# Kernel tuning notes

Measured on AMD Instinct MI355X. Metric: run time of the kernel, lower is better.

Reference implementation:

```python
import jax, jax.numpy as jnp
import numpy as np

N_EMBED = 1024
HIDDEN = int(2 / 3 * 4 * N_EMBED)  # 2730, matches SwiGLU default
NUM_EXPERTS = 8
TOP_K = 2


def setup_inputs() -> dict:
    key = jax.random.key(0)
    ks = jax.random.split(key, 5)
    B, T, C, E, H = 2, 2048, N_EMBED, NUM_EXPERTS, HIDDEN
    s = 0.02
    return {
        "x": jax.random.normal(ks[0], (B, T, C), dtype=jnp.float32),
        "gate_w": jax.random.normal(ks[1], (E, C), dtype=jnp.float32) * s,  # Linear(C->E) weight [out,in]
        "w1": jax.random.normal(ks[2], (E, H, C), dtype=jnp.float32) * s,   # per-expert Linear(C->H)
        "w2": jax.random.normal(ks[3], (E, H, C), dtype=jnp.float32) * s,   # per-expert Linear(C->H)
        "w3": jax.random.normal(ks[4], (E, C, H), dtype=jnp.float32) * s,   # per-expert Linear(H->C)
    }


def reference(x, gate_w, w1, w2, w3):
    B, T, C = x.shape
    E = gate_w.shape[0]
    xt = x.reshape(-1, C)                      # [N, C], N = B*T
    N = xt.shape[0]

    # Router: top-k logits, softmax over the selected logits only
    logits = jnp.einsum("nc,ec->ne", xt, gate_w)          # [N, E]
    top_vals, top_idx = jax.lax.top_k(logits, TOP_K)       # [N, K]
    top_w = jax.nn.softmax(top_vals.astype(jnp.float32), axis=-1).astype(x.dtype)

    # Dense routing-weight matrix [N, E] (top-k indices are distinct per token)
    route = jnp.zeros((N, E), dtype=x.dtype)
    route = route.at[jnp.arange(N)[:, None], top_idx].set(top_w)

    # SwiGLU for all experts, batched over the expert axis (faithful math,
    # vectorized instead of the per-expert Python-loop gather/scatter)
    h1 = jnp.einsum("nc,ehc->enh", xt, w1)                 # [E, N, H]
    h2 = jnp.einsum("nc,ehc->enh", xt, w2)                 # [E, N, H]
    act = jax.nn.silu(h1) * h2                              # [E, N, H]
    expert_out = jnp.einsum("enh,ech->enc", act, w3)       # [E, N, C]

    out = jnp.einsum("ne,enc->nc", route, expert_out)      # weighted combine
    return out.reshape(B, T, C)
```

## Files before the change

kernel.cpp:

```cpp
#include <hip/hip_runtime.h>
#include <hip/hip_bf16.h>
#include <cstdint>
#include <cstddef>

#define TOKENS 4096
#define CDIM   1024
#define HDIM   2730
#define HPAD2  2816
#define NEXP   8
#define NPAIR  (TOKENS * 2)
#define NTB1   (HPAD2 / 128)
#define NTB2   (CDIM / 256)
#define NT1    (CDIM / 64)
#define NT2    (HPAD2 / 64)
#define NCONV3 256

typedef __bf16 bf16_t;
typedef bf16_t bf16x8 __attribute__((ext_vector_type(8)));
typedef float  f32x4  __attribute__((ext_vector_type(4)));

static __device__ __forceinline__ unsigned short f2bf(float f) {
    union { float f; unsigned int u; } v; v.f = f;
    unsigned int u = v.u;
    return (unsigned short)((u + 0x7FFFu + ((u >> 16) & 1u)) >> 16);
}
static __device__ __forceinline__ unsigned int pack2(float a, float b) {
    return (unsigned int)f2bf(a) | ((unsigned int)f2bf(b) << 16);
}

typedef __attribute__((address_space(3))) unsigned int lds_uint;
typedef const __attribute__((address_space(1))) unsigned int glob_uint;
static __device__ __forceinline__ void gl_lds16(const void* g, void* l) {
    __builtin_amdgcn_global_load_lds((glob_uint*)g, (lds_uint*)l, 16, 0, 0);
}


__global__ __launch_bounds__(256) void moe_router_zero(
    const float* __restrict__ x, const float* __restrict__ gw,
    int* __restrict__ meta, int* __restrict__ tok_idx, float* __restrict__ tok_w,
    float* __restrict__ out)
{
    if (blockIdx.x >= 1024) {
        int b = blockIdx.x - 1024;
        float4 z4 = {0.f, 0.f, 0.f, 0.f};
#pragma unroll
        for (int i = 0; i < 4; ++i)
            ((float4*)out)[(size_t)b * 1024 + i * 256 + threadIdx.x] = z4;
        return;
    }
    int wave = threadIdx.x >> 6;
    int lane = threadIdx.x & 63;
    int t = blockIdx.x * 4 + wave;

    float acc[NEXP];
#pragma unroll
    for (int e = 0; e < NEXP; ++e) acc[e] = 0.f;

    const float4* xr = (const float4*)(x + (size_t)t * CDIM);
#pragma unroll
    for (int it = 0; it < 4; ++it) {
        int c4 = it * 64 + lane;
        float4 xv = xr[c4];
#pragma unroll
        for (int e = 0; e < NEXP; ++e) {
            float4 gv = ((const float4*)(gw + e * CDIM))[c4];
            acc[e] += xv.x * gv.x + xv.y * gv.y + xv.z * gv.z + xv.w * gv.w;
        }
    }
#pragma unroll
    for (int e = 0; e < NEXP; ++e) {
#pragma unroll
        for (int off = 32; off > 0; off >>= 1)
            acc[e] += __shfl_xor(acc[e], off, 64);
    }
    if (lane == 0) {
        int e0 = 0; float v0 = acc[0];
#pragma unroll
        for (int e = 1; e < NEXP; ++e) if (acc[e] > v0) { v0 = acc[e]; e0 = e; }
        int e1 = -1; float v1 = -3.0e38f;
#pragma unroll
        for (int e = 0; e < NEXP; ++e) if (e != e0 && acc[e] > v1) { v1 = acc[e]; e1 = e; }
        float w0 = 1.f / (1.f + __expf(v1 - v0));
        tok_idx[2 * t] = e0; tok_idx[2 * t + 1] = e1;
        tok_w[2 * t] = w0;  tok_w[2 * t + 1] = 1.f - w0;
        atomicAdd(&meta[e0], 1);
        atomicAdd(&meta[e1], 1);
    }
}

__global__ void moe_scan(int* meta) {
    if (threadIdx.x == 0) {
        int s = 0;
        for (int e = 0; e < NEXP; ++e) { meta[8 + e] = s; s += meta[e]; }
        meta[16] = s;
        int nb1 = 0;
        for (int e = 0; e < NEXP; ++e) {
            int beg = meta[8 + e], end = meta[8 + e] + meta[e];
            for (int m0 = beg; m0 < end; m0 += 256) {
                meta[32 + 2 * nb1] = e;
                meta[33 + 2 * nb1] = m0;
                ++nb1;
            }
        }
        meta[17] = nb1;
    }
}

__global__ __launch_bounds__(256) void moe_scatter(
    const int* __restrict__ tok_idx, const float* __restrict__ tok_w, int* meta,
    int* __restrict__ pair_token, float* __restrict__ pair_w)
{
    int t = blockIdx.x * 256 + threadIdx.x;
    if (t >= TOKENS) return;
#pragma unroll
    for (int k = 0; k < 2; ++k) {
        int e = tok_idx[2 * t + k];
        int pos = atomicAdd(&meta[24 + e], 1);
        int slot = meta[8 + e] + pos;
        pair_token[slot] = t;
        pair_w[slot] = tok_w[2 * t + k];
    }
}

__global__ __launch_bounds__(256) void moe_gather_conv12(
    const float* __restrict__ x, const int* __restrict__ pair_token,
    unsigned short* __restrict__ Xg,
    const float* __restrict__ w1, const float* __restrict__ w2,
    unsigned short* __restrict__ w1b, unsigned short* __restrict__ w2b)
{
    if (blockIdx.x < 1024) {
        int base = blockIdx.x * 8;
        int i = threadIdx.x;
#pragma unroll
        for (int r = 0; r < 8; ++r) {
            int row = base + r;
            int t = pair_token[row];
            float4 v = ((const float4*)(x + (size_t)t * CDIM))[i];
            ushort4 o;
            o.x = f2bf(v.x); o.y = f2bf(v.y); o.z = f2bf(v.z); o.w = f2bf(v.w);
            ((ushort4*)(Xg + (size_t)row * CDIM))[i] = o;
        }
        return;
    }
    int zz = blockIdx.x - 1024;
    int which = zz / 2816;
    int rr = zz - which * 2816;
    int e = rr / 352;
    int blk = rr - e * 352;
    const float* wsrc = which ? w2 : w1;
    unsigned short* wdst = which ? w2b : w1b;
    int half = threadIdx.x >> 7;
    int col = (threadIdx.x & 127) * 8;
#pragma unroll
    for (int r = 0; r < 4; ++r) {
        int row = blk * 8 + r * 2 + half;
        unsigned short* dst = wdst + ((size_t)e * HPAD2 + row) * CDIM;
        uint4 pv;
        if (row < HDIM) {
            const float* src = wsrc + ((size_t)e * HDIM + row) * CDIM + col;
            float4 a = *(const float4*)(src);
            float4 b = *(const float4*)(src + 4);
            pv.x = pack2(a.x, a.y); pv.y = pack2(a.z, a.w);
            pv.z = pack2(b.x, b.y); pv.w = pack2(b.z, b.w);
        } else {
            pv = uint4{0, 0, 0, 0};
        }
        *(uint4*)(dst + col) = pv;
    }
}

#define SWZ(row, ch) (((row) << 6) + ((((ch) ^ ((row) & 7))) << 3))

__global__ __launch_bounds__(512, 2) void moe_gemm1(
    const unsigned short* __restrict__ Xg,
    const unsigned short* __restrict__ w1b, const unsigned short* __restrict__ w2b,
    const float* __restrict__ pair_w, int* __restrict__ meta,
    unsigned short* __restrict__ act,
    const float* __restrict__ w3, unsigned short* __restrict__ w3b)
{
    __shared__ unsigned short sA[2][256 * 64];
    __shared__ unsigned short sB[2][256 * 64];
    __shared__ int sTile;

    int tid = threadIdx.x;
    int lane = tid & 63;
    int wv = tid >> 6;
    int wm = wv >> 2, wn = wv & 3;
    int l3 = lane >> 3;
    int l15 = lane & 15, l4 = lane >> 4;
    int srcc = (((lane & 7) ^ l3) << 3);

    int ntile = meta[17] * NTB1;

    for (;;) {
        if (tid == 0) sTile = atomicAdd(&meta[18], 1);
        __syncthreads();
        int t = sTile;
        if (t >= ntile + NCONV3) break;

        if (t >= ntile) {
            int c = t - ntile;
            int grow = c * 32 + (tid >> 4);
            int lanec = tid & 15;
            const float* src = w3 + (size_t)grow * HDIM;
            unsigned short* dst = w3b + (size_t)grow * HPAD2;
#pragma unroll
            for (int k = 0; k < 22; ++k) {
                int h = (lanec + k * 16) * 8;
                uint4 pv;
                if (h + 8 <= HDIM) {
                    float2 a = *(const float2*)(src + h);
                    float2 b = *(const float2*)(src + h + 2);
                    float2 c2 = *(const float2*)(src + h + 4);
                    float2 d = *(const float2*)(src + h + 6);
                    pv.x = pack2(a.x, a.y); pv.y = pack2(b.x, b.y);
                    pv.z = pack2(c2.x, c2.y); pv.w = pack2(d.x, d.y);
                } else if (h < HDIM) {
                    float v[8];
#pragma unroll
                    for (int q = 0; q < 8; ++q) v[q] = (h + q < HDIM) ? src[h + q] : 0.f;
                    pv.x = pack2(v[0], v[1]); pv.y = pack2(v[2], v[3]);
                    pv.z = pack2(v[4], v[5]); pv.w = pack2(v[6], v[7]);
                } else {
                    pv = uint4{0, 0, 0, 0};
                }
                *(uint4*)(dst + h) = pv;
            }
            continue;
        }

        int bm = t / NTB1, bn = t - bm * NTB1;
        int e  = meta[32 + 2 * bm];
        int m0 = meta[33 + 2 * bm];
        int mEnd = meta[9 + e];
        int mEndm1 = mEnd - 1;
        int n0 = bn * 128;

        const unsigned short* w1e = w1b + (size_t)e * HPAD2 * CDIM + (size_t)n0 * CDIM;
        const unsigned short* w2e = w2b + (size_t)e * HPAD2 * CDIM + (size_t)n0 * CDIM;
        const unsigned short* bbase = (wv < 4) ? w1e : w2e;

        f32x4 acc1[8][2], acc2[8][2];
#pragma unroll
        for (int i = 0; i < 8; ++i)
#pragma unroll
            for (int j = 0; j < 2; ++j) {
                acc1[i][j] = {0.f, 0.f, 0.f, 0.f};
                acc2[i][j] = {0.f, 0.f, 0.f, 0.f};
            }

        auto STAGE_A = [&](int b, int kk) {
            int k0 = kk * 64;
#pragma unroll
            for (int i_ = 0; i_ < 4; ++i_) {
                int seg = wv * 4 + i_;
                int arow = seg * 8 + l3;
                int grow = m0 + arow; if (grow > mEndm1) grow = mEndm1;
                gl_lds16(Xg + (size_t)grow * CDIM + k0 + srcc, sA[b] + seg * 512);
            }
        };
        auto STAGE_B = [&](int b, int kk) {
            int k0 = kk * 64;
#pragma unroll
            for (int i_ = 0; i_ < 4; ++i_) {
                int seg = wv * 4 + i_;
                int bseg = (wv < 4) ? seg : seg - 16;
                gl_lds16(bbase + (size_t)(bseg * 8 + l3) * CDIM + k0 + srcc, sB[b] + seg * 512);
            }
        };

        STAGE_A(0, 0); STAGE_B(0, 0);
        STAGE_A(1, 1); STAGE_B(1, 1);
        asm volatile("s_waitcnt vmcnt(8)" ::: "memory");
        __builtin_amdgcn_s_barrier();

        for (int t_ = 0; t_ < NT1; ++t_) {
            int cur = t_ & 1;
            const unsigned short* A = sA[cur];
            const unsigned short* B = sB[cur];
            bf16x8 af[2][4], b1f[2][2], b2f[2][2];

#pragma unroll
            for (int ks = 0; ks < 2; ++ks) {
                int kch = ks * 4 + l4;
#pragma unroll
                for (int i = 0; i < 4; ++i)
                    af[ks][i] = *(const bf16x8*)(A + SWZ(wm * 128 + i * 16 + l15, kch));
#pragma unroll
                for (int j = 0; j < 2; ++j)
                    b1f[ks][j] = *(const bf16x8*)(B + SWZ(wn * 32 + j * 16 + l15, kch));
            }
            __builtin_amdgcn_s_barrier();
            asm volatile("s_waitcnt lgkmcnt(0)" ::: "memory");
            __builtin_amdgcn_s_setprio(1);
#pragma unroll
            for (int ks = 0; ks < 2; ++ks)
#pragma unroll
                for (int i = 0; i < 4; ++i)
#pragma unroll
                    for (int j = 0; j < 2; ++j)
                        acc1[i][j] = __builtin_amdgcn_mfma_f32_16x16x32_bf16(af[ks][i], b1f[ks][j], acc1[i][j], 0, 0, 0);
            __builtin_amdgcn_s_setprio(0);
            __builtin_amdgcn_s_barrier();

#pragma unroll
            for (int ks = 0; ks < 2; ++ks) {
                int kch = ks * 4 + l4;
#pragma unroll
                for (int j = 0; j < 2; ++j)
                    b2f[ks][j] = *(const bf16x8*)(B + SWZ(128 + wn * 32 + j * 16 + l15, kch));
            }
            __builtin_amdgcn_s_barrier();
            asm volatile("s_waitcnt lgkmcnt(0)" ::: "memory");
            __builtin_amdgcn_s_setprio(1);
#pragma unroll
            for (int ks = 0; ks < 2; ++ks)
#pragma unroll
                for (int i = 0; i < 4; ++i)
#pragma unroll
                    for (int j = 0; j < 2; ++j)
                        acc2[i][j] = __builtin_amdgcn_mfma_f32_16x16x32_bf16(af[ks][i], b2f[ks][j], acc2[i][j], 0, 0, 0);
            __builtin_amdgcn_s_setprio(0);
            __builtin_amdgcn_s_barrier();

#pragma unroll
            for (int ks = 0; ks < 2; ++ks) {
                int kch = ks * 4 + l4;
#pragma unroll
                for (int i = 0; i < 4; ++i)
                    af[ks][i] = *(const bf16x8*)(A + SWZ(wm * 128 + 64 + i * 16 + l15, kch));
            }
            if (t_ + 2 < NT1) STAGE_B(cur, t_ + 2);
            __builtin_amdgcn_s_barrier();
            asm volatile("s_waitcnt lgkmcnt(0)" ::: "memory");
            __builtin_amdgcn_s_setprio(1);
#pragma unroll
            for (int ks = 0; ks < 2; ++ks)
#pragma unroll
                for (int i = 0; i < 4; ++i)
#pragma unroll
                    for (int j = 0; j < 2; ++j)
                        acc1[4 + i][j] = __builtin_amdgcn_mfma_f32_16x16x32_bf16(af[ks][i], b1f[ks][j], acc1[4 + i][j], 0, 0, 0);
            __builtin_amdgcn_s_setprio(0);
            __builtin_amdgcn_s_barrier();

            if (t_ + 2 < NT1) {
                STAGE_A(cur, t_ + 2);
                asm volatile("s_waitcnt vmcnt(8)" ::: "memory");
            } else {
                asm volatile("s_waitcnt vmcnt(0)" ::: "memory");
            }
            __builtin_amdgcn_s_barrier();
            __builtin_amdgcn_s_setprio(1);
#pragma unroll
            for (int ks = 0; ks < 2; ++ks)
#pragma unroll
                for (int i = 0; i < 4; ++i)
#pragma unroll
                    for (int j = 0; j < 2; ++j)
                        acc2[4 + i][j] = __builtin_amdgcn_mfma_f32_16x16x32_bf16(af[ks][i], b2f[ks][j], acc2[4 + i][j], 0, 0, 0);
            __builtin_amdgcn_s_setprio(0);
            __builtin_amdgcn_s_barrier();
        }

#pragma unroll
        for (int i = 0; i < 8; ++i) {
            int rbase = m0 + wm * 128 + ((i & 3) * 16) + ((i >> 2) * 64) + (l4 << 2);
#pragma unroll
            for (int r = 0; r < 4; ++r) {
                int grow = rbase + r;
                if (grow >= mEnd) continue;
                float pw = pair_w[grow];
                size_t rowoff = (size_t)grow * HPAD2;
#pragma unroll
                for (int j = 0; j < 2; ++j) {
                    int gcol = n0 + wn * 32 + j * 16 + l15;
                    int ai = (i & 3) + ((i >> 2) << 2);
                    float h1 = acc1[ai][j][r], h2 = acc2[ai][j][r];
                    float a = (h1 / (1.f + __expf(-h1))) * h2 * pw;
                    act[rowoff + gcol] = f2bf(a);
                }
            }
        }
    }
}

__global__ __launch_bounds__(512, 2) void moe_gemm2(
    const unsigned short* __restrict__ act,
    const unsigned short* __restrict__ w3b,
    int* __restrict__ meta, const int* __restrict__ pair_token,
    float* __restrict__ out)
{
    __shared__ unsigned short sA[2][256 * 64];
    __shared__ unsigned short sB[2][256 * 64];
    __shared__ int sTile;

    int tid = threadIdx.x;
    int lane = tid & 63;
    int wv = tid >> 6;
    int wm = wv >> 2, wn = wv & 3;
    int l3 = lane >> 3;
    int l15 = lane & 15, l4 = lane >> 4;
    int srcc = (((lane & 7) ^ l3) << 3);

    int ntile = meta[17] * NTB2;

    for (;;) {
        if (tid == 0) sTile = atomicAdd(&meta[19], 1);
        __syncthreads();
        int t = sTile;
        if (t >= ntile) break;

        int bm = t >> 2, bn = t & 3;
        int e  = meta[32 + 2 * bm];
        int m0 = meta[33 + 2 * bm];
        int mEnd = meta[9 + e];
        int mEndm1 = mEnd - 1;
        int n0 = bn * 256;

        const unsigned short* w3e = w3b + (size_t)e * CDIM * HPAD2 + (size_t)n0 * HPAD2;

        f32x4 acc[8][4];
#pragma unroll
        for (int i = 0; i < 8; ++i)
#pragma unroll
            for (int j = 0; j < 4; ++j) acc[i][j] = {0.f, 0.f, 0.f, 0.f};

        auto STAGE = [&](int b, int kk) {
            int k0 = kk * 64;
#pragma unroll
            for (int i_ = 0; i_ < 4; ++i_) {
                int seg = wv * 4 + i_;
                int row = seg * 8 + l3;
                int grow = m0 + row; if (grow > mEndm1) grow = mEndm1;
                gl_lds16(act + (size_t)grow * HPAD2 + k0 + srcc, sA[b] + seg * 512);
                gl_lds16(w3e + (size_t)row * HPAD2 + k0 + srcc, sB[b] + seg * 512);
            }
        };

        STAGE(0, 0);
        __syncthreads();
        for (int t_ = 0; t_ < NT2; ++t_) {
            int cur = t_ & 1;
            if (t_ + 1 < NT2) STAGE(cur ^ 1, t_ + 1);
#pragma unroll
            for (int ks = 0; ks < 2; ++ks) {
                int kch = ks * 4 + l4;
                bf16x8 af[8], bf[4];
#pragma unroll
                for (int i = 0; i < 8; ++i)
                    af[i] = *(const bf16x8*)(sA[cur] + SWZ(wm * 128 + i * 16 + l15, kch));
#pragma unroll
                for (int j = 0; j < 4; ++j)
                    bf[j] = *(const bf16x8*)(sB[cur] + SWZ(wn * 64 + j * 16 + l15, kch));
#pragma unroll
                for (int i = 0; i < 8; ++i)
#pragma unroll
                    for (int j = 0; j < 4; ++j)
                        acc[i][j] = __builtin_amdgcn_mfma_f32_16x16x32_bf16(af[i], bf[j], acc[i][j], 0, 0, 0);
            }
            __syncthreads();
        }

#pragma unroll
        for (int i = 0; i < 8; ++i) {
            int rbase = m0 + wm * 128 + i * 16 + (l4 << 2);
#pragma unroll
            for (int r = 0; r < 4; ++r) {
                int grow = rbase + r;
                if (grow >= mEnd) continue;
                int tok = pair_token[grow];
                float* orow = out + (size_t)tok * CDIM;
#pragma unroll
                for (int j = 0; j < 4; ++j) {
                    int gcol = n0 + wn * 64 + j * 16 + l15;
                    atomicAdd(orow + gcol, acc[i][j][r]);
                }
            }
        }
    }
}

extern "C" void kernel_launch(void* const* d_in, const int* in_sizes, int n_in,
                              void* d_out, int out_size, void* d_ws, size_t ws_size,
                              hipStream_t stream)
{
    const float* x  = (const float*)d_in[0];
    const float* gw = (const float*)d_in[1];
    const float* w1 = (const float*)d_in[2];
    const float* w2 = (const float*)d_in[3];
    const float* w3 = (const float*)d_in[4];
    float* out = (float*)d_out;

    char* ws = (char*)d_ws;
    size_t off = 0;
    auto alloc = [&](size_t bytes) -> void* {
        off = (off + 255) & ~(size_t)255;
        void* p = ws + off;
        off += bytes;
        return p;
    };
    int*   meta       = (int*)alloc(512 * sizeof(int));
    int*   tok_idx    = (int*)alloc((size_t)NPAIR * sizeof(int));
    float* tok_w      = (float*)alloc((size_t)NPAIR * sizeof(float));
    int*   pair_token = (int*)alloc((size_t)NPAIR * sizeof(int));
    float* pair_w     = (float*)alloc((size_t)NPAIR * sizeof(float));
    unsigned short* Xg  = (unsigned short*)alloc((size_t)NPAIR * CDIM * 2);
    unsigned short* act = (unsigned short*)alloc((size_t)NPAIR * HPAD2 * 2);
    unsigned short* w1b = (unsigned short*)alloc((size_t)NEXP * HPAD2 * CDIM * 2);
    unsigned short* w2b = (unsigned short*)alloc((size_t)NEXP * HPAD2 * CDIM * 2);
    unsigned short* w3b = (unsigned short*)alloc((size_t)NEXP * CDIM * HPAD2 * 2);
    (void)ws_size; (void)in_sizes; (void)n_in; (void)out_size;

    hipMemsetAsync(meta, 0, 512 * sizeof(int), stream);
    moe_router_zero<<<2048, 256, 0, stream>>>(x, gw, meta, tok_idx, tok_w, out);
    moe_scan<<<1, 64, 0, stream>>>(meta);
    moe_scatter<<<TOKENS / 256, 256, 0, stream>>>(tok_idx, tok_w, meta, pair_token, pair_w);
    moe_gather_conv12<<<1024 + 5632, 256, 0, stream>>>(x, pair_token, Xg, w1, w2, w1b, w2b);
    moe_gemm1<<<256, 512, 0, stream>>>(Xg, w1b, w2b, pair_w, meta, act, w3, w3b);
    moe_gemm2<<<256, 512, 0, stream>>>(act, w3b, meta, pair_token, out);
}
```

Baseline: 507.5 us.

## Replace gemm1 fine-grained ping-pong schedule with simple double buffer and stagger k-order

Drops the hand-scheduled gemm1 main loop, which used four barrier-separated MFMA phases, setprio and a two-deep prefetch. In its place is a plain double-buffered loop: prefetch the next k-tile, then run all MFMAs for both weight matrices per k-substep, with one __syncthreads per tile. In both GEMMs, odd waves now walk the two k-substeps in reverse order, intended to spread LDS bank conflicts and MFMA contention across waves. The change reduces barrier overhead but loses the finer-grained interleaving of loads and compute and the deeper prefetch, and it raises register pressure by holding 8 A fragments at once.

New measurement: 542.3 us. +6.9%, slower.

```diff
diff --git a/kernel.cpp b/kernel.cpp
--- a/kernel.cpp
+++ b/kernel.cpp
@@ -189,6 +189,7 @@
     int l3 = lane >> 3;
     int l15 = lane & 15, l4 = lane >> 4;
     int srcc = (((lane & 7) ^ l3) << 3);
+    int kpar = wv & 1;
 
     int ntile = meta[17] * NTB1;
 
@@ -249,7 +250,7 @@
                 acc2[i][j] = {0.f, 0.f, 0.f, 0.f};
             }
 
-        auto STAGE_A = [&](int b, int kk) {
+        auto STAGE = [&](int b, int kk) {
             int k0 = kk * 64;
 #pragma unroll
             for (int i_ = 0; i_ < 4; ++i_) {
@@ -257,115 +258,46 @@
                 int arow = seg * 8 + l3;
                 int grow = m0 + arow; if (grow > mEndm1) grow = mEndm1;
                 gl_lds16(Xg + (size_t)grow * CDIM + k0 + srcc, sA[b] + seg * 512);
-            }
-        };
-        auto STAGE_B = [&](int b, int kk) {
-            int k0 = kk * 64;
-#pragma unroll
-            for (int i_ = 0; i_ < 4; ++i_) {
-                int seg = wv * 4 + i_;
                 int bseg = (wv < 4) ? seg : seg - 16;
                 gl_lds16(bbase + (size_t)(bseg * 8 + l3) * CDIM + k0 + srcc, sB[b] + seg * 512);
             }
         };
 
-        STAGE_A(0, 0); STAGE_B(0, 0);
-        STAGE_A(1, 1); STAGE_B(1, 1);
-        asm volatile("s_waitcnt vmcnt(8)" ::: "memory");
-        __builtin_amdgcn_s_barrier();
-
+        STAGE(0, 0);
+        __syncthreads();
         for (int t_ = 0; t_ < NT1; ++t_) {
             int cur = t_ & 1;
-            const unsigned short* A = sA[cur];
-            const unsigned short* B = sB[cur];
-            bf16x8 af[2][4], b1f[2][2], b2f[2][2];
-
-#pragma unroll
-            for (int ks = 0; ks < 2; ++ks) {
+            if (t_ + 1 < NT1) STAGE(cur ^ 1, t_ + 1);
+#pragma unroll
+            for (int ks2 = 0; ks2 < 2; ++ks2) {
+                int ks = ks2 ^ kpar;
                 int kch = ks * 4 + l4;
-#pragma unroll
-                for (int i = 0; i < 4; ++i)
-                    af[ks][i] = *(const bf16x8*)(A + SWZ(wm * 128 + i * 16 + l15, kch));
-#pragma unroll
-                for (int j = 0; j < 2; ++j)
-                    b1f[ks][j] = *(const bf16x8*)(B + SWZ(wn * 32 + j * 16 + l15, kch));
-            }
-            __builtin_amdgcn_s_barrier();
-            asm volatile("s_waitcnt lgkmcnt(0)" ::: "memory");
-            __builtin_amdgcn_s_setprio(1);
-#pragma unroll
-            for (int ks = 0; ks < 2; ++ks)
-#pragma unroll
-                for (int i = 0; i < 4; ++i)
-#pragma unroll
-                    for (int j = 0; j < 2; ++j)
-                        acc1[i][j] = __builtin_amdgcn_mfma_f32_16x16x32_bf16(af[ks][i], b1f[ks][j], acc1[i][j], 0, 0, 0);
-            __builtin_amdgcn_s_setprio(0);
-            __builtin_amdgcn_s_barrier();
-
-#pragma unroll
-            for (int ks = 0; ks < 2; ++ks) {
-                int kch = ks * 4 + l4;
-#pragma unroll
-                for (int j = 0; j < 2; ++j)
-                    b2f[ks][j] = *(const bf16x8*)(B + SWZ(128 + wn * 32 + j * 16 + l15, kch));
-            }
-            __builtin_amdgcn_s_barrier();
-            asm volatile("s_waitcnt lgkmcnt(0)" ::: "memory");
-            __builtin_amdgcn_s_setprio(1);
-#pragma unroll
-            for (int ks = 0; ks < 2; ++ks)
-#pragma unroll
-                for (int i = 0; i < 4; ++i)
-#pragma unroll
-                    for (int j = 0; j < 2; ++j)
-                        acc2[i][j] = __builtin_amdgcn_mfma_f32_16x16x32_bf16(af[ks][i], b2f[ks][j], acc2[i][j], 0, 0, 0);
-            __builtin_amdgcn_s_setprio(0);
-            __builtin_amdgcn_s_barrier();
-
-#pragma unroll
-            for (int ks = 0; ks < 2; ++ks) {
-                int kch = ks * 4 + l4;
-#pragma unroll
-                for (int i = 0; i < 4; ++i)
-                    af[ks][i] = *(const bf16x8*)(A + SWZ(wm * 128 + 64 + i * 16 + l15, kch));
-            }
-            if (t_ + 2 < NT1) STAGE_B(cur, t_ + 2);
-            __builtin_amdgcn_s_barrier();
-            asm volatile("s_waitcnt lgkmcnt(0)" ::: "memory");
-            __builtin_amdgcn_s_setprio(1);
-#pragma unroll
-            for (int ks = 0; ks < 2; ++ks)
-#pragma unroll
-                for (int i = 0; i < 4; ++i)
-#pragma unroll
-                    for (int j = 0; j < 2; ++j)
-                        acc1[4 + i][j] = __builtin_amdgcn_mfma_f32_16x16x32_bf16(af[ks][i], b1f[ks][j], acc1[4 + i][j], 0, 0, 0);
-            __builtin_amdgcn_s_setprio(0);
-            __builtin_amdgcn_s_barrier();
-
-            if (t_ + 2 < NT1) {
-                STAGE_A(cur, t_ + 2);
-                asm volatile("s_waitcnt vmcnt(8)" ::: "memory");
-            } else {
-                asm volatile("s_waitcnt vmcnt(0)" ::: "memory");
-            }
-            __builtin_amdgcn_s_barrier();
-            __builtin_amdgcn_s_setprio(1);
-#pragma unroll
-            for (int ks = 0; ks < 2; ++ks)
-#pragma unroll
-                for (int i = 0; i < 4; ++i)
-#pragma unroll
-                    for (int j = 0; j < 2; ++j)
-                        acc2[4 + i][j] = __builtin_amdgcn_mfma_f32_16x16x32_bf16(af[ks][i], b2f[ks][j], acc2[4 + i][j], 0, 0, 0);
-            __builtin_amdgcn_s_setprio(0);
-            __builtin_amdgcn_s_barrier();
+                bf16x8 af[8], b1f[2], b2f[2];
+#pragma unroll
+                for (int i = 0; i < 8; ++i) {
+                    int r = wm * 128 + i * 16 + l15;
+                    af[i] = *(const bf16x8*)(sA[cur] + SWZ(r, kch));
+                }
+#pragma unroll
+                for (int j = 0; j < 2; ++j) {
+                    int r1 = wn * 32 + j * 16 + l15;
+                    b1f[j] = *(const bf16x8*)(sB[cur] + SWZ(r1, kch));
+                    b2f[j] = *(const bf16x8*)(sB[cur] + SWZ(128 + r1, kch));
+                }
+#pragma unroll
+                for (int i = 0; i < 8; ++i)
+#pragma unroll
+                    for (int j = 0; j < 2; ++j) {
+                        acc1[i][j] = __builtin_amdgcn_mfma_f32_16x16x32_bf16(af[i], b1f[j], acc1[i][j], 0, 0, 0);
+                        acc2[i][j] = __builtin_amdgcn_mfma_f32_16x16x32_bf16(af[i], b2f[j], acc2[i][j], 0, 0, 0);
+                    }
+            }
+            __syncthreads();
         }
 
 #pragma unroll
         for (int i = 0; i < 8; ++i) {
-            int rbase = m0 + wm * 128 + ((i & 3) * 16) + ((i >> 2) * 64) + (l4 << 2);
+            int rbase = m0 + wm * 128 + i * 16 + (l4 << 2);
 #pragma unroll
             for (int r = 0; r < 4; ++r) {
                 int grow = rbase + r;
@@ -375,8 +307,7 @@
 #pragma unroll
                 for (int j = 0; j < 2; ++j) {
                     int gcol = n0 + wn * 32 + j * 16 + l15;
-                    int ai = (i & 3) + ((i >> 2) << 2);
-                    float h1 = acc1[ai][j][r], h2 = acc2[ai][j][r];
+                    float h1 = acc1[i][j][r], h2 = acc2[i][j][r];
                     float a = (h1 / (1.f + __expf(-h1))) * h2 * pw;
                     act[rowoff + gcol] = f2bf(a);
                 }
@@ -402,6 +333,7 @@
     int l3 = lane >> 3;
     int l15 = lane & 15, l4 = lane >> 4;
     int srcc = (((lane & 7) ^ l3) << 3);
+    int kpar = wv & 1;
 
     int ntile = meta[17] * NTB2;
 
@@ -444,7 +376,8 @@
             int cur = t_ & 1;
             if (t_ + 1 < NT2) STAGE(cur ^ 1, t_ + 1);
 #pragma unroll
-            for (int ks = 0; ks < 2; ++ks) {
+            for (int ks2 = 0; ks2 < 2; ++ks2) {
+                int ks = ks2 ^ kpar;
                 int kch = ks * 4 + l4;
                 bf16x8 af[8], bf[4];
 #pragma unroll
```
